# Kernel tuning notes

Hardware: AMD Instinct MI355X
Metric: run time of the kernel (lower is better)

The kernel has to match this reference:

```python
import jax, jax.numpy as jnp
import numpy as np
from jax import lax

B, D, N, C = 8, 1, 12288, 256
H = 8            # num_heads
WS = 64          # window size (pixels per window)
HID = 1024       # mlp hidden = 4*C
K = 9            # conv kernel size
EPS = 1e-5


def setup_inputs() -> dict:
    key = jax.random.key(0)
    ks = jax.random.split(key, 8)
    w = lambda i, shape: jax.random.normal(ks[i], shape, jnp.float32) * 0.02
    return {
        "x": jax.random.normal(ks[0], (B, D, N, C), jnp.float32),
        "ln1_g": jnp.ones((C,), jnp.float32),
        "ln1_b": jnp.zeros((C,), jnp.float32),
        "conv_w": w(1, (C, C, K)),            # OIH layout (out_ch, in_ch, k)
        "conv_b": jnp.zeros((C,), jnp.float32),
        "qkv_w": w(2, (C, 3 * C)),            # stored (in, out): y = x @ W + b
        "qkv_b": jnp.zeros((3 * C,), jnp.float32),
        "proj_w": w(3, (C, C)),
        "proj_b": jnp.zeros((C,), jnp.float32),
        "ln2_g": jnp.ones((C,), jnp.float32),
        "ln2_b": jnp.zeros((C,), jnp.float32),
        "fc1_w": w(4, (C, HID)),
        "fc1_b": jnp.zeros((HID,), jnp.float32),
        "fc2_w": w(5, (HID, C)),
        "fc2_b": jnp.zeros((C,), jnp.float32),
    }


def _layernorm(x, g, b):
    mu = jnp.mean(x, axis=-1, keepdims=True)
    var = jnp.mean(jnp.square(x - mu), axis=-1, keepdims=True)
    return (x - mu) * lax.rsqrt(var + EPS) * g + b


def reference(x, ln1_g, ln1_b, conv_w, conv_b, qkv_w, qkv_b,
              proj_w, proj_b, ln2_g, ln2_b, fc1_w, fc1_b, fc2_w, fc2_b):
    shortcut = x                                  # (B, D, N, C)
    h = _layernorm(x, ln1_g, ln1_b)

    # Conv1d over pixel dim N, channels C, same padding
    hc = h.reshape(B * D, N, C).transpose(0, 2, 1)            # (BD, C, N)
    hc = lax.conv_general_dilated(
        hc, conv_w, window_strides=(1,), padding=[((K - 1) // 2, (K - 1) // 2)],
        dimension_numbers=("NCH", "OIH", "NCH"))
    hc = hc + conv_b[None, :, None]
    h = hc.transpose(0, 2, 1).reshape(B, D, N, C)

    # Window partition (no shift): (B*D*N/WS, WS, C)
    win = h.reshape(-1, WS, C)
    hd = C // H
    qkv = (win @ qkv_w + qkv_b).reshape(-1, WS, 3, H, hd)
    q = qkv[:, :, 0].transpose(0, 2, 1, 3)        # (nW, H, WS, hd)
    k = qkv[:, :, 1].transpose(0, 2, 1, 3)
    v = qkv[:, :, 2].transpose(0, 2, 1, 3)
    scale = hd ** (-0.5)
    attn = jnp.einsum("whqd,whkd->whqk", q * scale, k)
    attn = jax.nn.softmax(attn, axis=-1)
    out = jnp.einsum("whqk,whkd->whqd", attn, v)
    out = out.transpose(0, 2, 1, 3).reshape(-1, WS, C)
    out = out @ proj_w + proj_b

    h = out.reshape(B, D, N, C)
    x1 = shortcut + h                             # residual 1
    mlp_in = _layernorm(x1, ln2_g, ln2_b)
    mlp = jax.nn.gelu(mlp_in @ fc1_w + fc1_b, approximate=False) @ fc2_w + fc2_b
    return x1 + mlp                               # residual 2
```

## Files before the change

kernel.cpp:

```cpp
#include <hip/hip_runtime.h>

#define DEVI __device__ __forceinline__

typedef __attribute__((ext_vector_type(4))) float  f32x4;
typedef __attribute__((ext_vector_type(8))) short  s16x8;
typedef __attribute__((ext_vector_type(4))) short  s16x4;
typedef __attribute__((ext_vector_type(8))) __bf16 bf16x8;

constexpr int  Nn  = 12288;
constexpr int  NP  = 12296;
constexpr long TOK = 98304;

DEVI short f2bf(float f) {
  unsigned u = __builtin_bit_cast(unsigned, f);
  u += 0x7fffu + ((u >> 16) & 1u);
  return (short)(u >> 16);
}

DEVI float fast_gelu(float v) {
  const float a = 1.5957691216f * (v + 0.044715f * v * v * v);
  return v / (1.0f + __expf(-a));
}

DEVI f32x4 MFMA(s16x8 a, s16x8 b, f32x4 c) {
  return __builtin_amdgcn_mfma_f32_16x16x32_bf16(
      __builtin_bit_cast(bf16x8, a), __builtin_bit_cast(bf16x8, b), c, 0, 0, 0);
}

DEVI void gld16(const void* g, void* l) {
  __builtin_amdgcn_global_load_lds(
      (const __attribute__((address_space(1))) void*)g,
      (__attribute__((address_space(3))) void*)l, 16, 0, 0);
}

template <int CNT, int NT>
DEVI void stageG(const short* __restrict__ g_base, long g_row0, int ld, int k0,
                 short* __restrict__ lds, int tid) {
  const int w = tid >> 6;
#pragma unroll
  for (int c = 0; c < CNT; ++c) {
    const int u = c * NT + tid;
    const int row = u >> 3, ch = u & 7;
    const short* g = g_base + (g_row0 + row) * (long)ld + k0 + ch * 8;
    gld16(g, lds + (c * NT + w * 64) * 8);
  }
}

DEVI void xcd_decode(int W, int total, int ncol, long& row0, int& col0) {
  const int per = total >> 3;
  const int L = (W & 7) * per + (W >> 3);
  row0 = (long)(L / ncol) * 128;
  col0 = (L % ncol) * 128;
}

__global__ void prep_k(const float* __restrict__ qkv_w, const float* __restrict__ proj_w,
                       const float* __restrict__ fc1_w, const float* __restrict__ fc2_w,
                       const float* __restrict__ conv_w,
                       short* __restrict__ qkvWt, short* __restrict__ projWt,
                       short* __restrict__ fc1Wt, short* __restrict__ fc2Wt,
                       short* __restrict__ convWt, short* __restrict__ hp) {
  int idx = blockIdx.x * 256 + threadIdx.x;
  if (idx < 196608) {
    int o = idx >> 8, i = idx & 255;
    qkvWt[idx] = f2bf(qkv_w[i * 768 + o]);
    return;
  }
  idx -= 196608;
  if (idx < 65536) {
    int o = idx >> 8, i = idx & 255;
    projWt[idx] = f2bf(proj_w[i * 256 + o]);
    return;
  }
  idx -= 65536;
  if (idx < 262144) {
    int o = idx >> 8, i = idx & 255;
    fc1Wt[idx] = f2bf(fc1_w[i * 1024 + o]);
    return;
  }
  idx -= 262144;
  if (idx < 262144) {
    int o = idx >> 10, i = idx & 1023;
    fc2Wt[idx] = f2bf(fc2_w[i * 256 + o]);
    return;
  }
  idx -= 262144;
  if (idx < 589824) {
    int co = idx / 2304, rem = idx % 2304;
    int k = rem >> 8, ci = rem & 255;
    convWt[idx] = f2bf(conv_w[co * 2304 + ci * 9 + k]);
    return;
  }
  idx -= 589824;
  if (idx < 16384) {
    int b = idx >> 11, rem = idx & 2047;
    int rs = rem >> 8, ch = rem & 255;
    int p = rs < 4 ? rs : 12288 + rs;
    hp[((long)b * NP + p) * 256 + ch] = 0;
  }
}

__global__ __launch_bounds__(256) void ln_k(const float* __restrict__ x,
                                            const float* __restrict__ gw,
                                            const float* __restrict__ bw,
                                            short* __restrict__ out) {
  const int tid = threadIdx.x, w = tid >> 6, lane = tid & 63;
  const long t = (long)blockIdx.x * 4 + w;
  f32x4 v = *((const f32x4*)(x + t * 256) + lane);
  float s  = v[0] + v[1] + v[2] + v[3];
  float ss = v[0] * v[0] + v[1] * v[1] + v[2] * v[2] + v[3] * v[3];
#pragma unroll
  for (int mk = 1; mk < 64; mk <<= 1) {
    s  += __shfl_xor(s, mk);
    ss += __shfl_xor(ss, mk);
  }
  const float mu   = s * (1.0f / 256.0f);
  const float var  = ss * (1.0f / 256.0f) - mu * mu;
  const float rstd = rsqrtf(var + 1e-5f);
  f32x4 g4 = *((const f32x4*)gw + lane);
  f32x4 b4 = *((const f32x4*)bw + lane);
  const long orow = t + (t / Nn) * 8 + 4;
  s16x4 o4;
#pragma unroll
  for (int j = 0; j < 4; ++j) o4[j] = f2bf((v[j] - mu) * rstd * g4[j] + b4[j]);
  *((s16x4*)(out + orow * 256) + lane) = o4;
}

template <int EPI>
__global__ __launch_bounds__(256, 2) void gemm_k(
    const short* __restrict__ A, int lda,
    const short* __restrict__ Bt,
    const float* __restrict__ bias,
    const float* res, short* outS, float* outF,
    int ldo, int K, int ncol) {
  __shared__ __align__(16) short As[128][64];
  __shared__ __align__(16) short Bs[128][64];
  const int tid = threadIdx.x, w = tid >> 6, lane = tid & 63;
  const int q = lane >> 4, r16 = lane & 15;
  long row0; int col0;
  xcd_decode(blockIdx.x, gridDim.x, ncol, row0, col0);
  const int wr = w >> 1, wc = w & 1;
  f32x4 acc[4][4] = {};

  for (int k0 = 0; k0 < K; k0 += 64) {
    stageG<4, 256>(A, row0, lda, k0, &As[0][0], tid);
    stageG<4, 256>(Bt, col0, K, k0, &Bs[0][0], tid);
    __syncthreads();
#pragma unroll
    for (int kk = 0; kk < 2; ++kk) {
      s16x8 af[4], bfv[4];
#pragma unroll
      for (int m = 0; m < 4; ++m) af[m] = *(const s16x8*)&As[wr * 64 + m * 16 + r16][kk * 32 + q * 8];
#pragma unroll
      for (int n = 0; n < 4; ++n) bfv[n] = *(const s16x8*)&Bs[wc * 64 + n * 16 + r16][kk * 32 + q * 8];
#pragma unroll
      for (int m = 0; m < 4; ++m)
#pragma unroll
        for (int n = 0; n < 4; ++n) acc[m][n] = MFMA(af[m], bfv[n], acc[m][n]);
    }
    __syncthreads();
  }

  const long orow = row0 + wr * 64;
  const int  ocol = col0 + wc * 64;
#pragma unroll
  for (int n = 0; n < 4; ++n) {
    const int   gc = ocol + n * 16 + r16;
    const float bn = bias[gc];
#pragma unroll
    for (int m = 0; m < 4; ++m) {
      const long gr = orow + m * 16 + q * 4;
#pragma unroll
      for (int r = 0; r < 4; ++r) {
        float v = acc[m][n][r] + bn;
        const long o = (gr + r) * (long)ldo + gc;
        if constexpr (EPI == 0) {
          outS[o] = f2bf(v);
        } else if constexpr (EPI == 1) {
          outF[o] = v + res[o];
        } else {
          outS[o] = f2bf(fast_gelu(v));
        }
      }
    }
  }
}

__global__ __launch_bounds__(256, 2) void conv_k(const short* __restrict__ hp,
                                                 const short* __restrict__ convWt,
                                                 const float* __restrict__ bias,
                                                 short* __restrict__ out) {
  __shared__ __align__(16) short As[160][64];
  __shared__ __align__(16) short Bs[2][128][64];
  const int tid = threadIdx.x, w = tid >> 6, lane = tid & 63;
  const int q = lane >> 4, r16 = lane & 15;
  long row0; int col0;
  xcd_decode(blockIdx.x, gridDim.x, 2, row0, col0);
  const int  b  = (int)(row0 / Nn);
  const int  n0 = (int)(row0 % Nn);
  const long abase = (long)b * NP + n0;
  const int  wr = w >> 1, wc = w & 1;
  f32x4 acc[4][4] = {};

  stageG<5, 256>(hp, abase, 256, 0, &As[0][0], tid);
  stageG<4, 256>(convWt, col0, 2304, 0, &Bs[0][0][0], tid);
  __syncthreads();
  int cur = 0;
  for (int k0 = 0; k0 < 256; k0 += 64) {
    for (int tap = 0; tap < 9; ++tap) {
      if (tap < 8)
        stageG<4, 256>(convWt, col0, 2304, (tap + 1) * 256 + k0, &Bs[cur ^ 1][0][0], tid);
      else if (k0 + 64 < 256)
        stageG<4, 256>(convWt, col0, 2304, k0 + 64, &Bs[cur ^ 1][0][0], tid);
#pragma unroll
      for (int kk = 0; kk < 2; ++kk) {
        s16x8 af[4], bfv[4];
#pragma unroll
        for (int m = 0; m < 4; ++m)
          af[m] = *(const s16x8*)&As[tap + wr * 64 + m * 16 + r16][kk * 32 + q * 8];
#pragma unroll
        for (int n = 0; n < 4; ++n)
          bfv[n] = *(const s16x8*)&Bs[cur][wc * 64 + n * 16 + r16][kk * 32 + q * 8];
#pragma unroll
        for (int m = 0; m < 4; ++m)
#pragma unroll
          for (int n = 0; n < 4; ++n) acc[m][n] = MFMA(af[m], bfv[n], acc[m][n]);
      }
      __syncthreads();
      cur ^= 1;
    }
    if (k0 + 64 < 256) {
      stageG<5, 256>(hp, abase, 256, k0 + 64, &As[0][0], tid);
      __syncthreads();
    }
  }

  const long orow = row0 + wr * 64;
  const int  ocol = col0 + wc * 64;
#pragma unroll
  for (int n = 0; n < 4; ++n) {
    const int   gc = ocol + n * 16 + r16;
    const float bn = bias[gc];
#pragma unroll
    for (int m = 0; m < 4; ++m) {
      const long gr = orow + m * 16 + q * 4;
#pragma unroll
      for (int r = 0; r < 4; ++r) out[(gr + r) * 256L + gc] = f2bf(acc[m][n][r] + bn);
    }
  }
}

__global__ __launch_bounds__(512, 4) void proj_ln_k(
    const short* __restrict__ A,
    const short* __restrict__ Bt,
    const float* __restrict__ bias,
    const float* __restrict__ res,
    const float* __restrict__ gw, const float* __restrict__ bw,
    float* __restrict__ x1,
    short* __restrict__ lnout) {
  __shared__ __align__(16) short As[128][64];
  __shared__ __align__(16) short Bs[256][64];
  __shared__ float red[4][128][2];
  const int tid = threadIdx.x, w = tid >> 6, lane = tid & 63;
  const int q = lane >> 4, r16 = lane & 15;
  const int W = blockIdx.x, per = gridDim.x >> 3;
  const long row0 = (long)((W & 7) * per + (W >> 3)) * 128;
  const int wr = w >> 2, wc = w & 3;
  f32x4 acc[4][4] = {};

  for (int k0 = 0; k0 < 256; k0 += 64) {
    stageG<2, 512>(A, row0, 256, k0, &As[0][0], tid);
    stageG<4, 512>(Bt, 0, 256, k0, &Bs[0][0], tid);
    __syncthreads();
#pragma unroll
    for (int kk = 0; kk < 2; ++kk) {
      s16x8 af[4], bfv[4];
#pragma unroll
      for (int m = 0; m < 4; ++m) af[m] = *(const s16x8*)&As[wr * 64 + m * 16 + r16][kk * 32 + q * 8];
#pragma unroll
      for (int n = 0; n < 4; ++n) bfv[n] = *(const s16x8*)&Bs[wc * 64 + n * 16 + r16][kk * 32 + q * 8];
#pragma unroll
      for (int m = 0; m < 4; ++m)
#pragma unroll
        for (int n = 0; n < 4; ++n) acc[m][n] = MFMA(af[m], bfv[n], acc[m][n]);
    }
    __syncthreads();
  }

  float biasr[4], gv[4], bv[4];
#pragma unroll
  for (int n = 0; n < 4; ++n) {
    const int gc = wc * 64 + n * 16 + r16;
    biasr[n] = bias[gc]; gv[n] = gw[gc]; bv[n] = bw[gc];
  }

#pragma unroll
  for (int m = 0; m < 4; ++m) {
#pragma unroll
    for (int r = 0; r < 4; ++r) {
      const long gr = row0 + wr * 64 + m * 16 + q * 4 + r;
      float s = 0.f, ss = 0.f;
#pragma unroll
      for (int n = 0; n < 4; ++n) {
        const int gc = wc * 64 + n * 16 + r16;
        float v = acc[m][n][r] + biasr[n] + res[gr * 256 + gc];
        acc[m][n][r] = v;
        x1[gr * 256 + gc] = v;
        s += v; ss += v * v;
      }
#pragma unroll
      for (int mk = 1; mk < 16; mk <<= 1) {
        s  += __shfl_xor(s, mk);
        ss += __shfl_xor(ss, mk);
      }
      if (r16 == 0) {
        const int lr = wr * 64 + m * 16 + q * 4 + r;
        red[wc][lr][0] = s;
        red[wc][lr][1] = ss;
      }
    }
  }
  __syncthreads();

#pragma unroll
  for (int m = 0; m < 4; ++m) {
#pragma unroll
    for (int r = 0; r < 4; ++r) {
      const int  lr = wr * 64 + m * 16 + q * 4 + r;
      const long gr = row0 + lr;
      const float S  = red[0][lr][0] + red[1][lr][0] + red[2][lr][0] + red[3][lr][0];
      const float SS = red[0][lr][1] + red[1][lr][1] + red[2][lr][1] + red[3][lr][1];
      const float mu = S * (1.0f / 256.0f);
      const float rstd = rsqrtf(SS * (1.0f / 256.0f) - mu * mu + 1e-5f);
#pragma unroll
      for (int n = 0; n < 4; ++n) {
        const int gc = wc * 64 + n * 16 + r16;
        lnout[gr * 256 + gc] = f2bf((acc[m][n][r] - mu) * rstd * gv[n] + bv[n]);
      }
    }
  }
}

__global__ __launch_bounds__(256, 2) void attn_k(const short* __restrict__ qkv,
                                                 short* __restrict__ o) {
  __shared__ __align__(16) short Pt[4][64][68];
  __shared__ __align__(16) short Vs[4][64][32];
  const int tid = threadIdx.x, w = tid >> 6, lane = tid & 63;
  const int q = lane >> 4, r16 = lane & 15;
  const int job = blockIdx.x * 4 + w;
  const int win = job >> 3, h = job & 7;
  const short* base = qkv + (long)win * 64 * 768;

#pragma unroll
  for (int c = 0; c < 4; ++c) {
    const int idx16 = c * 64 + lane;
    const short* g = base + (long)(idx16 >> 2) * 768 + 512 + h * 32 + (idx16 & 3) * 8;
    gld16(g, (char*)&Vs[w][0][0] + c * 1024);
  }

  s16x8 aq[4], bk[4];
#pragma unroll
  for (int m = 0; m < 4; ++m)
    aq[m] = *(const s16x8*)(base + (long)(m * 16 + r16) * 768 + h * 32 + q * 8);
#pragma unroll
  for (int n = 0; n < 4; ++n)
    bk[n] = *(const s16x8*)(base + (long)(n * 16 + r16) * 768 + 256 + h * 32 + q * 8);
  f32x4 sc[4][4] = {};
#pragma unroll
  for (int m = 0; m < 4; ++m)
#pragma unroll
    for (int n = 0; n < 4; ++n) sc[m][n] = MFMA(aq[m], bk[n], sc[m][n]);

  const float scale = 0.17677669529663687f;
#pragma unroll
  for (int m = 0; m < 4; ++m) {
#pragma unroll
    for (int r = 0; r < 4; ++r) {
      float a0 = sc[m][0][r] * scale, a1 = sc[m][1][r] * scale;
      float a2 = sc[m][2][r] * scale, a3 = sc[m][3][r] * scale;
      float mx = fmaxf(fmaxf(a0, a1), fmaxf(a2, a3));
      mx = fmaxf(mx, __shfl_xor(mx, 1));
      mx = fmaxf(mx, __shfl_xor(mx, 2));
      mx = fmaxf(mx, __shfl_xor(mx, 4));
      mx = fmaxf(mx, __shfl_xor(mx, 8));
      float e0 = __expf(a0 - mx), e1 = __expf(a1 - mx);
      float e2 = __expf(a2 - mx), e3 = __expf(a3 - mx);
      float sm = e0 + e1 + e2 + e3;
      sm += __shfl_xor(sm, 1);
      sm += __shfl_xor(sm, 2);
      sm += __shfl_xor(sm, 4);
      sm += __shfl_xor(sm, 8);
      float inv = 1.0f / sm;
      sc[m][0][r] = e0 * inv; sc[m][1][r] = e1 * inv;
      sc[m][2][r] = e2 * inv; sc[m][3][r] = e3 * inv;
    }
  }

#pragma unroll
  for (int m = 0; m < 4; ++m)
#pragma unroll
    for (int n = 0; n < 4; ++n) {
      s16x4 p4;
#pragma unroll
      for (int r = 0; r < 4; ++r) p4[r] = f2bf(sc[m][n][r]);
      *(s16x4*)&Pt[w][n * 16 + r16][m * 16 + q * 4] = p4;
    }

  asm volatile("s_waitcnt vmcnt(0)" ::: "memory");

  f32x4 oa[4][2] = {};
#pragma unroll
  for (int ks = 0; ks < 2; ++ks) {
    s16x8 bv[2];
#pragma unroll
    for (int nt = 0; nt < 2; ++nt)
#pragma unroll
      for (int jj = 0; jj < 8; ++jj)
        bv[nt][jj] = Vs[w][ks * 32 + q * 8 + jj][nt * 16 + r16];
#pragma unroll
    for (int m = 0; m < 4; ++m) {
      s16x8 ap;
#pragma unroll
      for (int jj = 0; jj < 8; ++jj)
        ap[jj] = Pt[w][ks * 32 + q * 8 + jj][m * 16 + r16];
#pragma unroll
      for (int nt = 0; nt < 2; ++nt) oa[m][nt] = MFMA(ap, bv[nt], oa[m][nt]);
    }
  }

  short* ob = o + (long)win * 64 * 256 + h * 32;
#pragma unroll
  for (int m = 0; m < 4; ++m)
#pragma unroll
    for (int nt = 0; nt < 2; ++nt)
#pragma unroll
      for (int r = 0; r < 4; ++r)
        ob[(long)(m * 16 + q * 4 + r) * 256 + nt * 16 + r16] = f2bf(oa[m][nt][r]);
}

extern "C" void kernel_launch(void* const* d_in, const int* in_sizes, int n_in,
                              void* d_out, int out_size, void* d_ws, size_t ws_size,
                              hipStream_t stream) {
  const float* x      = (const float*)d_in[0];
  const float* ln1_g  = (const float*)d_in[1];
  const float* ln1_b  = (const float*)d_in[2];
  const float* conv_w = (const float*)d_in[3];
  const float* conv_b = (const float*)d_in[4];
  const float* qkv_w  = (const float*)d_in[5];
  const float* qkv_b  = (const float*)d_in[6];
  const float* proj_w = (const float*)d_in[7];
  const float* proj_b = (const float*)d_in[8];
  const float* ln2_g  = (const float*)d_in[9];
  const float* ln2_b  = (const float*)d_in[10];
  const float* fc1_w  = (const float*)d_in[11];
  const float* fc1_b  = (const float*)d_in[12];
  const float* fc2_w  = (const float*)d_in[13];
  const float* fc2_b  = (const float*)d_in[14];
  float* out = (float*)d_out;

  constexpr long HPsz = (long)8 * NP * 256;
  constexpr long Qsz  = TOK * 768;
  constexpr long Csz  = TOK * 256;
  short* ws    = (short*)d_ws;
  short* hp    = ws;
  short* qkvB  = ws + HPsz;
  short* cvB   = ws + HPsz + Qsz;
  short* hidB  = qkvB;
  short* wts   = ws + HPsz + Qsz + Csz;
  short* qkvWt  = wts;
  short* projWt = qkvWt + 196608;
  short* fc1Wt  = projWt + 65536;
  short* fc2Wt  = fc1Wt + 262144;
  short* convWt = fc2Wt + 262144;

  prep_k<<<5440, 256, 0, stream>>>(qkv_w, proj_w, fc1_w, fc2_w, conv_w,
                                   qkvWt, projWt, fc1Wt, fc2Wt, convWt, hp);
  ln_k<<<24576, 256, 0, stream>>>(x, ln1_g, ln1_b, hp);
  conv_k<<<1536, 256, 0, stream>>>(hp, convWt, conv_b, cvB);
  gemm_k<0><<<4608, 256, 0, stream>>>(cvB, 256, qkvWt, qkv_b,
                                      nullptr, qkvB, nullptr, 768, 256, 6);
  attn_k<<<3072, 256, 0, stream>>>(qkvB, hp);
  proj_ln_k<<<768, 512, 0, stream>>>(hp, projWt, proj_b, x, ln2_g, ln2_b, out, hp);
  gemm_k<2><<<6144, 256, 0, stream>>>(hp, 256, fc1Wt, fc1_b,
                                      nullptr, hidB, nullptr, 1024, 256, 8);
  gemm_k<1><<<1536, 256, 0, stream>>>(hidB, 1024, fc2Wt, fc2_b,
                                      out, nullptr, out, 256, 1024, 2);
}
```

Baseline: 651.3 us.

## Add persistent-B GEMM keeping full K=256 weight slice resident in LDS

Adds gemmR_k, which loads a 128x256 weight slice into LDS once per block and loops over 8 row tiles of 128, restaging only the A tiles. Both A and B tiles use XOR-swizzled LDS layouts to avoid bank conflicts. It replaces the QKV and fc1 GEMM launches with far fewer blocks, aiming to cut redundant weight loads and launch overhead. In exchange it uses 80KB of LDS per block, which limits occupancy, and the inner loop has no double buffering, so global loads are not overlapped with MFMA work.

```diff
diff --git a/kernel.cpp b/kernel.cpp
--- a/kernel.cpp
+++ b/kernel.cpp
@@ -43,6 +43,30 @@
     const int row = u >> 3, ch = u & 7;
     const short* g = g_base + (g_row0 + row) * (long)ld + k0 + ch * 8;
     gld16(g, lds + (c * NT + w * 64) * 8);
+  }
+}
+
+DEVI void stageA_sw(const short* __restrict__ g, long row0, int lda, int k0,
+                    short* __restrict__ lds, int tid) {
+#pragma unroll
+  for (int c = 0; c < 4; ++c) {
+    const int u = c * 256 + tid;
+    const int row = u >> 3, slot = u & 7;
+    const int ch = slot ^ (row & 7);
+    gld16(g + (row0 + row) * (long)lda + k0 + ch * 8,
+          lds + (c * 256 + (tid >> 6) * 64) * 8);
+  }
+}
+
+DEVI void stageB_sw(const short* __restrict__ g, int col0,
+                    short* __restrict__ lds, int tid) {
+#pragma unroll
+  for (int c = 0; c < 16; ++c) {
+    const int u = c * 256 + tid;
+    const int row = u >> 5, slot = u & 31;
+    const int ch = (slot & 24) | ((slot & 7) ^ (row & 7));
+    gld16(g + (long)(col0 + row) * 256 + ch * 8,
+          lds + (c * 256 + (tid >> 6) * 64) * 8);
   }
 }
 
@@ -123,6 +147,75 @@
 #pragma unroll
   for (int j = 0; j < 4; ++j) o4[j] = f2bf((v[j] - mu) * rstd * g4[j] + b4[j]);
   *((s16x4*)(out + orow * 256) + lane) = o4;
+}
+
+template <int EPI>
+__global__ __launch_bounds__(256, 2) void gemmR_k(
+    const short* __restrict__ A,
+    const short* __restrict__ Bt,
+    const float* __restrict__ bias,
+    short* __restrict__ outS,
+    int ldo, int nslice, int nrg) {
+  __shared__ __align__(16) short Bs[128 * 256];
+  __shared__ __align__(16) short As[128 * 64];
+  const int tid = threadIdx.x, w = tid >> 6, lane = tid & 63;
+  const int q = lane >> 4, r16 = lane & 15;
+  const int W = blockIdx.x, per = gridDim.x >> 3;
+  const int L = (W & 7) * per + (W >> 3);
+  const int slice = L % nslice, rg = L / nslice;
+  const int col0 = slice * 128;
+  const long rgbase = (long)rg * 1024;
+  const int wr = w >> 1, wc = w & 1;
+
+  stageB_sw(Bt, col0, Bs, tid);
+
+  for (int r = 0; r < 8; ++r) {
+    const long row0 = rgbase + r * 128;
+    f32x4 acc[4][4] = {};
+    for (int t = 0; t < 4; ++t) {
+      stageA_sw(A, row0, 256, t * 64, As, tid);
+      __syncthreads();
+#pragma unroll
+      for (int kkl = 0; kkl < 2; ++kkl) {
+        s16x8 af[4], bfv[4];
+#pragma unroll
+        for (int m = 0; m < 4; ++m) {
+          const int row = wr * 64 + m * 16 + r16;
+          const int ud = kkl * 4 + q;
+          af[m] = *(const s16x8*)(As + row * 64 + (ud ^ (row & 7)) * 8);
+        }
+#pragma unroll
+        for (int n = 0; n < 4; ++n) {
+          const int row = wc * 64 + n * 16 + r16;
+          const int ud = (t * 2 + kkl) * 4 + q;
+          const int slot = (ud & 24) | ((ud & 7) ^ (row & 7));
+          bfv[n] = *(const s16x8*)(Bs + row * 256 + slot * 8);
+        }
+#pragma unroll
+        for (int m = 0; m < 4; ++m)
+#pragma unroll
+          for (int n = 0; n < 4; ++n) acc[m][n] = MFMA(af[m], bfv[n], acc[m][n]);
+      }
+      __syncthreads();
+    }
+    const long orow = row0 + wr * 64;
+    const int  ocol = col0 + wc * 64;
+#pragma unroll
+    for (int n = 0; n < 4; ++n) {
+      const int   gc = ocol + n * 16 + r16;
+      const float bn = bias[gc];
+#pragma unroll
+      for (int m = 0; m < 4; ++m) {
+        const long gr = orow + m * 16 + q * 4;
+#pragma unroll
+        for (int rr = 0; rr < 4; ++rr) {
+          float v = acc[m][n][rr] + bn;
+          if constexpr (EPI == 2) v = fast_gelu(v);
+          outS[(gr + rr) * (long)ldo + gc] = f2bf(v);
+        }
+      }
+    }
+  }
 }
 
 template <int EPI>
@@ -476,12 +569,10 @@
                                    qkvWt, projWt, fc1Wt, fc2Wt, convWt, hp);
   ln_k<<<24576, 256, 0, stream>>>(x, ln1_g, ln1_b, hp);
   conv_k<<<1536, 256, 0, stream>>>(hp, convWt, conv_b, cvB);
-  gemm_k<0><<<4608, 256, 0, stream>>>(cvB, 256, qkvWt, qkv_b,
-                                      nullptr, qkvB, nullptr, 768, 256, 6);
+  gemmR_k<0><<<576, 256, 0, stream>>>(cvB, qkvWt, qkv_b, qkvB, 768, 6, 96);
   attn_k<<<3072, 256, 0, stream>>>(qkvB, hp);
   proj_ln_k<<<768, 512, 0, stream>>>(hp, projWt, proj_b, x, ln2_g, ln2_b, out, hp);
-  gemm_k<2><<<6144, 256, 0, stream>>>(hp, 256, fc1Wt, fc1_b,
-                                      nullptr, hidB, nullptr, 1024, 256, 8);
+  gemmR_k<2><<<768, 256, 0, stream>>>(hp, fc1Wt, fc1_b, hidB, 1024, 8, 96);
   gemm_k<1><<<1536, 256, 0, stream>>>(hidB, 1024, fc2Wt, fc2_b,
                                       out, nullptr, out, 256, 1024, 2);
 }
```

After: 685.6 us. +5.3%, slower.
